# Kernel optimization log

Hardware: AMD Instinct MI355X
Metric: run time of the kernel (lower is better)

Reference implementation:

```python
import jax, jax.numpy as jnp
import numpy as np

V, E, H, W, S, T, B = 10000, 256, 512, 256, 512, 128, 64


def setup_inputs() -> dict:
    key = jax.random.key(0)
    ks = jax.random.split(key, 17)
    def rn(k, shape, s=0.08):
        return jax.random.normal(k, shape, jnp.float32) * s
    return {
        "tokens": jax.random.randint(ks[0], (B, S), 0, V),
        "dec_h0": jax.random.normal(ks[1], (B, H), jnp.float32),
        "emb_table": rn(ks[2], (V, E), 1.0),
        "enc_Wih": rn(ks[3], (4 * H, E)),
        "enc_Whh": rn(ks[4], (4 * H, H)),
        "enc_bih": rn(ks[5], (4 * H,)),
        "enc_bhh": rn(ks[6], (4 * H,)),
        "dec_Wih": rn(ks[7], (4 * H, E)),
        "dec_Whh": rn(ks[8], (4 * H, H)),
        "dec_bih": rn(ks[9], (4 * H,)),
        "dec_bhh": rn(ks[10], (4 * H,)),
        "W1_w": rn(ks[11], (W, H)),
        "W1_b": rn(ks[12], (W,)),
        "W2_w": rn(ks[13], (W, H)),
        "W2_b": rn(ks[14], (W,)),
        "vt_w": rn(ks[15], (1, W)),
        "vt_b": rn(ks[16], (1,)),
    }


def _lstm_cell(x, h, c, Wih, Whh, bih, bhh):
    # PyTorch gate order: input, forget, cell(g), output
    gates = x @ Wih.T + h @ Whh.T + bih + bhh
    i, f, g, o = jnp.split(gates, 4, axis=-1)
    c = jax.nn.sigmoid(f) * c + jax.nn.sigmoid(i) * jnp.tanh(g)
    h = jax.nn.sigmoid(o) * jnp.tanh(c)
    return h, c


def reference(tokens, dec_h0, emb_table, enc_Wih, enc_Whh, enc_bih, enc_bhh,
              dec_Wih, dec_Whh, dec_bih, dec_bhh, W1_w, W1_b, W2_w, W2_b,
              vt_w, vt_b):
    emb = emb_table[tokens]                       # [B,S,E]
    x_sbe = jnp.swapaxes(emb, 0, 1)               # [S,B,E] time-major
    bsz = tokens.shape[0]
    h0 = jnp.zeros((bsz, enc_Whh.shape[1]), emb.dtype)

    def enc_step(carry, x):
        h, c = carry
        h, c = _lstm_cell(x, h, c, enc_Wih, enc_Whh, enc_bih, enc_bhh)
        return (h, c), h

    _, enc_states = jax.lax.scan(enc_step, (h0, h0), x_sbe)   # [S,B,H]

    # W1(encoder_states) is constant across decoder steps -> hoist it
    blend1 = enc_states @ W1_w.T + W1_b            # [S,B,W]
    c0 = enc_states[-1]                            # original uses last enc state as cell init
    dec_in = jnp.zeros((bsz, emb_table.shape[1]), emb.dtype)  # never updated in original

    def dec_step(carry, _):
        h, c = carry
        h, c = _lstm_cell(dec_in, h, c, dec_Wih, dec_Whh, dec_bih, dec_bhh)
        blend2 = h @ W2_w.T + W2_b                 # [B,W]
        u = (jnp.tanh(blend1 + blend2[None]) @ vt_w.T)[..., 0] + vt_b[0]  # [S,B]
        logp = jax.nn.log_softmax(u.T, axis=1)     # [B,S], softmax over seq positions
        return (h, c), logp

    _, probs = jax.lax.scan(dec_step, (dec_h0, c0), None, length=T)  # [T,B,S]
    return jnp.swapaxes(probs, 0, 1)               # [B,T,S]
```

## Files before the change

kernel.cpp:

```cpp
#include <hip/hip_runtime.h>
#include <hip/hip_bf16.h>
#include <cstdint>
#include <cstddef>

typedef __bf16 bf16_t;
typedef __bf16 bf16x8 __attribute__((ext_vector_type(8)));
typedef float  f32x4  __attribute__((ext_vector_type(4)));

#define NB 64
#define NS 512
#define NTD 128
#define NE 256
#define NH 512
#define NG 2048
#define NW 256

#define HSTEP_DW 16384u

__device__ __forceinline__ float sigm_f(float x) { return 1.f / (1.f + __expf(-x)); }
__device__ __forceinline__ float tanh_f(float x) {
  float e = __expf(2.f * x);
  return 1.f - 2.f / (e + 1.f);
}
__device__ __forceinline__ float bits2f(uint32_t b16) {
  uint32_t u = b16 << 16;
  return __builtin_bit_cast(float, u);
}
__device__ __forceinline__ uint32_t packh(float a, float b) {
  uint16_t lo = __builtin_bit_cast(uint16_t, (bf16_t)a);
  uint16_t hi = __builtin_bit_cast(uint16_t, (bf16_t)b);
  return (uint32_t)lo | ((uint32_t)hi << 16);
}
__device__ __forceinline__ uint32_t aload(const uint32_t* p) {
  return __hip_atomic_load(p, __ATOMIC_RELAXED, __HIP_MEMORY_SCOPE_AGENT);
}
__device__ __forceinline__ uint64_t aload64(const uint64_t* p) {
  return __hip_atomic_load(p, __ATOMIC_RELAXED, __HIP_MEMORY_SCOPE_AGENT);
}
__device__ __forceinline__ void astore(uint32_t* p, uint32_t v) {
  __hip_atomic_store(p, v, __ATOMIC_RELAXED, __HIP_MEMORY_SCOPE_AGENT);
}

__global__ __launch_bounds__(256) void pack_all(
    const float* __restrict__ s0, bf16_t* __restrict__ d0,
    const float* __restrict__ s1, bf16_t* __restrict__ d1,
    const float* __restrict__ s2, bf16_t* __restrict__ d2,
    const float* __restrict__ s3, bf16_t* __restrict__ d3,
    const float* __restrict__ s4, bf16_t* __restrict__ d4) {
  int blk = blockIdx.x;
  const float* src; bf16_t* dst; int K, idx;
  if (blk < 2048)       { src = s0; dst = d0; K = 256; idx = blk * 256 + threadIdx.x; }
  else if (blk < 6144)  { src = s1; dst = d1; K = 512; idx = (blk - 2048) * 256 + threadIdx.x; }
  else if (blk < 10240) { src = s2; dst = d2; K = 512; idx = (blk - 6144) * 256 + threadIdx.x; }
  else if (blk < 10752) { src = s3; dst = d3; K = 512; idx = (blk - 10240) * 256 + threadIdx.x; }
  else                  { src = s4; dst = d4; K = 512; idx = (blk - 10752) * 256 + threadIdx.x; }
  int n = idx / K, k = idx - n * K;
  int lane = (((k & 31) >> 3) << 4) | (n & 15);
  size_t o = ((((size_t)(n >> 4) * (K >> 5)) + (k >> 5)) * 64 + lane) * 8 + (k & 7);
  dst[o] = (bf16_t)src[idx];
}

__global__ __launch_bounds__(256) void gather_emb2(
    const int* __restrict__ tokens, const float* __restrict__ table,
    bf16_t* __restrict__ embfrag, const float* __restrict__ dec_h0,
    uint32_t* __restrict__ dec_hf0) {
  int blk = blockIdx.x;
  if (blk < 4096) {
    int idx = blk * 256 + threadIdx.x;
    int row = idx >> 5, e0 = (idx & 31) << 3;
    int b = row & 63, s = row >> 6;
    int tok = tokens[b * NS + s];
    const float4* p = (const float4*)(table + (size_t)tok * NE + e0);
    float4 v0 = p[0], v1 = p[1];
    bf16x8 v;
    v[0] = (bf16_t)v0.x; v[1] = (bf16_t)v0.y; v[2] = (bf16_t)v0.z; v[3] = (bf16_t)v0.w;
    v[4] = (bf16_t)v1.x; v[5] = (bf16_t)v1.y; v[6] = (bf16_t)v1.z; v[7] = (bf16_t)v1.w;
    int mt = row >> 4;
    int ks = e0 >> 5;
    int lane = (b & 15) | (((e0 >> 3) & 3) << 4);
    *(bf16x8*)(embfrag + ((size_t)(mt * 8 + ks) * 64 + lane) * 8) = v;
  } else {
    int idx = (blk - 4096) * 256 + threadIdx.x;
    int b = idx >> 8, jp = idx & 255;
    int j = jp * 2;
    float lo = dec_h0[(size_t)b * NH + j], hi = dec_h0[(size_t)b * NH + j + 1];
    int bg = b >> 4, bl = b & 15, ks = j >> 5;
    int lane = bl | (((j >> 3) & 3) << 4);
    dec_hf0[((size_t)bg * 16 + ks) * 256 + lane * 4 + ((j >> 1) & 3)] = packh(lo, hi);
  }
}

__global__ __launch_bounds__(256) void gemm_xih_st(const bf16_t* __restrict__ A,
                                                   const bf16_t* __restrict__ Bp,
                                                   bf16_t* __restrict__ out,
                                                   const float* __restrict__ b1,
                                                   const float* __restrict__ b2) {
  __shared__ bf16_t tile[16][68];
  const int KS = 8, MT = 16;
  int lane = threadIdx.x & 63, w = threadIdx.x >> 6;
  int nt = blockIdx.x * 4 + w;
  int mt0 = blockIdx.y * MT;
  bf16x8 bfr[KS];
  const bf16_t* bp = Bp + ((size_t)nt * KS * 64 + lane) * 8;
#pragma unroll
  for (int ks = 0; ks < KS; ++ks) bfr[ks] = *(const bf16x8*)(bp + (size_t)ks * 512);
  int col = (nt << 4) + (lane & 15);
  float bs = b1[col] + b2[col];
  int row0 = (lane >> 4) << 2;
  int rw = threadIdx.x >> 4, ch = threadIdx.x & 15;
  for (int m = 0; m < MT; ++m) {
    int mt = mt0 + m;
    const bf16_t* ap = A + (size_t)mt * (KS * 512) + lane * 8;
    f32x4 acc = {0.f, 0.f, 0.f, 0.f};
#pragma unroll
    for (int ks = 0; ks < KS; ++ks)
      acc = __builtin_amdgcn_mfma_f32_16x16x32_bf16(
          *(const bf16x8*)(ap + (size_t)ks * 512), bfr[ks], acc, 0, 0, 0);
#pragma unroll
    for (int r = 0; r < 4; ++r)
      tile[row0 + r][w * 16 + (lane & 15)] = (bf16_t)(acc[r] + bs);
    __syncthreads();
    ushort4 v = *(const ushort4*)&tile[rw][ch * 4];
    *(ushort4*)(out + (size_t)(mt * 16 + rw) * NG + blockIdx.x * 64 + ch * 4) = v;
    __syncthreads();
  }
}

__global__ __launch_bounds__(256) void gemm_blends(
    const bf16_t* __restrict__ encA, const bf16_t* __restrict__ W1p,
    const float* __restrict__ W1_b, bf16_t* __restrict__ blend1,
    const bf16_t* __restrict__ decA, const bf16_t* __restrict__ W2p,
    const float* __restrict__ W2_b, float* __restrict__ blend2) {
  union { bf16_t t16[16][68]; float t32[16][68]; } sm;
  __shared__ decltype(sm) tile;
  const int KS = 16;
  int lane = threadIdx.x & 63, w = threadIdx.x >> 6;
  int nt = blockIdx.x * 4 + w;
  bool is1 = blockIdx.y < 128;
  int mt0 = (is1 ? blockIdx.y : (blockIdx.y - 128)) * 16;
  const bf16_t* A  = is1 ? encA : decA;
  const bf16_t* Bp = is1 ? W1p : W2p;
  const float* bias = is1 ? W1_b : W2_b;
  bf16x8 bfr[KS];
  const bf16_t* bp = Bp + ((size_t)nt * KS * 64 + lane) * 8;
#pragma unroll
  for (int ks = 0; ks < KS; ++ks) bfr[ks] = *(const bf16x8*)(bp + (size_t)ks * 512);
  int col = (nt << 4) + (lane & 15);
  float bs = bias[col];
  int row0 = (lane >> 4) << 2;
  int rw = threadIdx.x >> 4, ch = threadIdx.x & 15;
  for (int m = 0; m < 16; ++m) {
    int mt = mt0 + m;
    const bf16_t* ap = A + (size_t)mt * (KS * 512) + lane * 8;
    f32x4 acc = {0.f, 0.f, 0.f, 0.f};
#pragma unroll
    for (int ks = 0; ks < KS; ++ks)
      acc = __builtin_amdgcn_mfma_f32_16x16x32_bf16(
          *(const bf16x8*)(ap + (size_t)ks * 512), bfr[ks], acc, 0, 0, 0);
    if (is1) {
#pragma unroll
      for (int r = 0; r < 4; ++r)
        tile.t16[row0 + r][w * 16 + (lane & 15)] = (bf16_t)(acc[r] + bs);
      __syncthreads();
      ushort4 v = *(const ushort4*)&tile.t16[rw][ch * 4];
      *(ushort4*)(blend1 + (size_t)(mt * 16 + rw) * NW + blockIdx.x * 64 + ch * 4) = v;
      __syncthreads();
    } else {
#pragma unroll
      for (int r = 0; r < 4; ++r)
        tile.t32[row0 + r][w * 16 + (lane & 15)] = acc[r] + bs;
      __syncthreads();
      float4 v = *(const float4*)&tile.t32[rw][ch * 4];
      *(float4*)(blend2 + (size_t)(mt * 16 + rw) * NW + blockIdx.x * 64 + ch * 4) = v;
      __syncthreads();
    }
  }
}

__global__ __launch_bounds__(256) void lstm_chain_enc(
    const bf16_t* __restrict__ Wp, const bf16_t* __restrict__ xih,
    uint32_t* __restrict__ hfrag, uint32_t* __restrict__ flags) {
  __shared__ bf16_t wlds[8 * 8192];
  __shared__ float gl[4][16][36];
  int tid = threadIdx.x, lane = tid & 63, wv = tid >> 6;
  int bg = blockIdx.x >> 4, slice = blockIdx.x & 15;

  for (int l = 0; l < 8; ++l) {
    int g = l >> 1, p = l & 1;
    const bf16_t* src = Wp + (size_t)(g * 32 + slice * 2 + p) * 8192;
    bf16_t* dst = wlds + (size_t)l * 8192;
    for (int i = tid; i < 1024; i += 256)
      *(bf16x8*)(dst + (size_t)i * 8) = *(const bf16x8*)(src + (size_t)i * 8);
  }

  int ub = tid >> 4, uj2 = tid & 15;
  int lane_f = ub | ((uj2 >> 2) << 4);
  float c0 = 0.f, c1 = 0.f;
  __syncthreads();

  const uint64_t* hq = (const uint64_t*)hfrag;
  uint32_t* fl = flags + bg * 16;

  for (int t = 0; t < NS; ++t) {
    uint32_t xd[4];
    {
      const uint32_t* xr = (const uint32_t*)xih +
          ((size_t)(t * 64 + bg * 16 + ub)) * 1024 + slice * 16 + uj2;
#pragma unroll
      for (int g = 0; g < 4; ++g) xd[g] = xr[(size_t)g * 256];
    }
    if (t > 0) {
      uint32_t tgt = (uint32_t)t;
      bool ok;
      do {
        uint32_t f = tgt;
        if (lane < 16 && lane != (uint32_t)slice) f = aload(fl + lane);
        ok = __all(f >= tgt);
      } while (!ok);
    }
    const uint64_t* hb = hq + ((size_t)t * 4 + bg) * 2048 + lane * 2;
    uint64_t aq[16][2];
#pragma unroll
    for (int ks = 0; ks < 16; ++ks) {
      aq[ks][0] = aload64(hb + (size_t)ks * 128);
      aq[ks][1] = aload64(hb + (size_t)ks * 128 + 1);
    }
    const bf16_t* wl = wlds + (size_t)(wv * 2) * 8192 + lane * 8;
    f32x4 acc0 = {0.f, 0.f, 0.f, 0.f}, acc1 = {0.f, 0.f, 0.f, 0.f};
#pragma unroll
    for (int ks = 0; ks < 16; ++ks) {
      union { uint64_t q[2]; bf16x8 v; } u;
      u.q[0] = aq[ks][0]; u.q[1] = aq[ks][1];
      acc0 = __builtin_amdgcn_mfma_f32_16x16x32_bf16(
          u.v, *(const bf16x8*)(wl + (size_t)ks * 512), acc0, 0, 0, 0);
      acc1 = __builtin_amdgcn_mfma_f32_16x16x32_bf16(
          u.v, *(const bf16x8*)(wl + 8192 + (size_t)ks * 512), acc1, 0, 0, 0);
    }
    int cc = lane & 15, rb = (lane >> 4) << 2;
#pragma unroll
    for (int r = 0; r < 4; ++r) {
      gl[wv][rb + r][cc] = acc0[r];
      gl[wv][rb + r][16 + cc] = acc1[r];
    }
    __syncthreads();

    float p[4][2];
#pragma unroll
    for (int g = 0; g < 4; ++g) {
      p[g][0] = gl[g][ub][uj2 * 2] + bits2f(xd[g] & 0xffffu);
      p[g][1] = gl[g][ub][uj2 * 2 + 1] + bits2f(xd[g] >> 16);
    }
    float i0 = sigm_f(p[0][0]), f0 = sigm_f(p[1][0]);
    float g0 = tanh_f(p[2][0]), o0 = sigm_f(p[3][0]);
    c0 = f0 * c0 + i0 * g0;
    float h0 = o0 * tanh_f(c0);
    float i1 = sigm_f(p[0][1]), f1 = sigm_f(p[1][1]);
    float g1 = tanh_f(p[2][1]), o1 = sigm_f(p[3][1]);
    c1 = f1 * c1 + i1 * g1;
    float h1 = o1 * tanh_f(c1);
    astore(hfrag + ((size_t)(t + 1) * 4 + bg) * 4096 +
               slice * 256 + lane_f * 4 + (uj2 & 3), packh(h0, h1));
    __syncthreads();
    if (tid == 0) astore(fl + slice, (uint32_t)(t + 1));
  }
}

__global__ __launch_bounds__(256) void lstm_chain_dec(
    const bf16_t* __restrict__ Wp, const float* __restrict__ bih,
    const float* __restrict__ bhh, uint32_t* __restrict__ hfrag,
    const uint32_t* __restrict__ c0frag, uint32_t* __restrict__ flags) {
  __shared__ bf16_t wlds[8 * 8192];
  __shared__ float gl[4][16][36];
  int tid = threadIdx.x, lane = tid & 63, wv = tid >> 6;
  int bg = blockIdx.x >> 4, slice = blockIdx.x & 15;

  for (int l = 0; l < 8; ++l) {
    int g = l >> 1, p = l & 1;
    const bf16_t* src = Wp + (size_t)(g * 32 + slice * 2 + p) * 8192;
    bf16_t* dst = wlds + (size_t)l * 8192;
    for (int i = tid; i < 1024; i += 256)
      *(bf16x8*)(dst + (size_t)i * 8) = *(const bf16x8*)(src + (size_t)i * 8);
  }
  int ub = tid >> 4, uj2 = tid & 15;
  int j_lo = slice * 32 + uj2 * 2;
  int lane_f = ub | ((uj2 >> 2) << 4);
  uint32_t d = c0frag[((size_t)bg * 16 + slice) * 256 + lane_f * 4 + (uj2 & 3)];
  float c0 = bits2f(d & 0xffffu), c1 = bits2f(d >> 16);
  float bsum[4][2];
#pragma unroll
  for (int g = 0; g < 4; ++g) {
    bsum[g][0] = bih[g * NH + j_lo] + bhh[g * NH + j_lo];
    bsum[g][1] = bih[g * NH + j_lo + 1] + bhh[g * NH + j_lo + 1];
  }
  __syncthreads();

  const uint64_t* hq = (const uint64_t*)hfrag;
  uint32_t* fl = flags + bg * 16;

  for (int t = 0; t < NTD; ++t) {
    if (t > 0) {
      uint32_t tgt = (uint32_t)t;
      bool ok;
      do {
        uint32_t f = tgt;
        if (lane < 16 && lane != (uint32_t)slice) f = aload(fl + lane);
        ok = __all(f >= tgt);
      } while (!ok);
    }
    const uint64_t* hb = hq + ((size_t)t * 4 + bg) * 2048 + lane * 2;
    uint64_t aq[16][2];
#pragma unroll
    for (int ks = 0; ks < 16; ++ks) {
      aq[ks][0] = aload64(hb + (size_t)ks * 128);
      aq[ks][1] = aload64(hb + (size_t)ks * 128 + 1);
    }
    const bf16_t* wl = wlds + (size_t)(wv * 2) * 8192 + lane * 8;
    f32x4 acc0 = {0.f, 0.f, 0.f, 0.f}, acc1 = {0.f, 0.f, 0.f, 0.f};
#pragma unroll
    for (int ks = 0; ks < 16; ++ks) {
      union { uint64_t q[2]; bf16x8 v; } u;
      u.q[0] = aq[ks][0]; u.q[1] = aq[ks][1];
      acc0 = __builtin_amdgcn_mfma_f32_16x16x32_bf16(
          u.v, *(const bf16x8*)(wl + (size_t)ks * 512), acc0, 0, 0, 0);
      acc1 = __builtin_amdgcn_mfma_f32_16x16x32_bf16(
          u.v, *(const bf16x8*)(wl + 8192 + (size_t)ks * 512), acc1, 0, 0, 0);
    }
    int cc = lane & 15, rb = (lane >> 4) << 2;
#pragma unroll
    for (int r = 0; r < 4; ++r) {
      gl[wv][rb + r][cc] = acc0[r];
      gl[wv][rb + r][16 + cc] = acc1[r];
    }
    __syncthreads();

    float p[4][2];
#pragma unroll
    for (int g = 0; g < 4; ++g) {
      p[g][0] = gl[g][ub][uj2 * 2] + bsum[g][0];
      p[g][1] = gl[g][ub][uj2 * 2 + 1] + bsum[g][1];
    }
    float i0 = sigm_f(p[0][0]), f0 = sigm_f(p[1][0]);
    float g0 = tanh_f(p[2][0]), o0 = sigm_f(p[3][0]);
    c0 = f0 * c0 + i0 * g0;
    float h0 = o0 * tanh_f(c0);
    float i1 = sigm_f(p[0][1]), f1 = sigm_f(p[1][1]);
    float g1 = tanh_f(p[2][1]), o1 = sigm_f(p[3][1]);
    c1 = f1 * c1 + i1 * g1;
    float h1 = o1 * tanh_f(c1);
    astore(hfrag + ((size_t)(t + 1) * 4 + bg) * 4096 +
               slice * 256 + lane_f * 4 + (uj2 & 3), packh(h0, h1));
    __syncthreads();
    if (tid == 0) astore(fl + slice, (uint32_t)(t + 1));
  }
}

__global__ __launch_bounds__(256) void attn_v2(const bf16_t* __restrict__ blend1,
                                               const float* __restrict__ blend2,
                                               const float* __restrict__ vt_w,
                                               float* __restrict__ out) {
  __shared__ float s_u[512], s_red[8];
  int t = blockIdx.x >> 6, b = blockIdx.x & 63;
  int tid = threadIdx.x, lane = tid & 63, wv = tid >> 6;
  int sslot = lane >> 4, wseg = lane & 15;
  int w0 = wseg * 16;

  float vt[16], b2[16];
  {
    const float4* vp = (const float4*)(vt_w + w0);
    const float4* bp = (const float4*)(blend2 + (size_t)(t * 64 + b) * NW + w0);
#pragma unroll
    for (int i = 0; i < 4; ++i) {
      float4 a = vp[i], c = bp[i];
      vt[i * 4 + 0] = a.x; vt[i * 4 + 1] = a.y; vt[i * 4 + 2] = a.z; vt[i * 4 + 3] = a.w;
      b2[i * 4 + 0] = c.x; b2[i * 4 + 1] = c.y; b2[i * 4 + 2] = c.z; b2[i * 4 + 3] = c.w;
    }
  }
  for (int p = 0; p < 32; ++p) {
    int s = p * 16 + wv * 4 + sslot;
    const bf16_t* row = blend1 + ((size_t)s * NB + b) * NW + w0;
    bf16x8 v0 = *(const bf16x8*)(row);
    bf16x8 v1 = *(const bf16x8*)(row + 8);
    float val = 0.f;
#pragma unroll
    for (int k = 0; k < 8; ++k) val += vt[k] * tanh_f((float)v0[k] + b2[k]);
#pragma unroll
    for (int k = 0; k < 8; ++k) val += vt[8 + k] * tanh_f((float)v1[k] + b2[8 + k]);
    val += __shfl_xor(val, 1, 64);
    val += __shfl_xor(val, 2, 64);
    val += __shfl_xor(val, 4, 64);
    val += __shfl_xor(val, 8, 64);
    if (wseg == 0) s_u[s] = val;
  }
  __syncthreads();
  float a = s_u[tid], bb2 = s_u[tid + 256];
  float m = fmaxf(a, bb2);
#pragma unroll
  for (int o = 1; o < 64; o <<= 1) m = fmaxf(m, __shfl_xor(m, o, 64));
  if (lane == 0) s_red[wv] = m;
  __syncthreads();
  m = fmaxf(fmaxf(s_red[0], s_red[1]), fmaxf(s_red[2], s_red[3]));
  float e = __expf(a - m) + __expf(bb2 - m);
#pragma unroll
  for (int o = 1; o < 64; o <<= 1) e += __shfl_xor(e, o, 64);
  if (lane == 0) s_red[4 + wv] = e;
  __syncthreads();
  float lz = m + logf(s_red[4] + s_red[5] + s_red[6] + s_red[7]);
  size_t ob = ((size_t)b * NTD + t) * NS;
  out[ob + tid] = a - lz;
  out[ob + tid + 256] = bb2 - lz;
}

extern "C" void kernel_launch(void* const* d_in, const int* in_sizes, int n_in,
                              void* d_out, int out_size, void* d_ws, size_t ws_size,
                              hipStream_t stream) {
  const int*   tokens    = (const int*)d_in[0];
  const float* dec_h0    = (const float*)d_in[1];
  const float* emb_table = (const float*)d_in[2];
  const float* enc_Wih   = (const float*)d_in[3];
  const float* enc_Whh   = (const float*)d_in[4];
  const float* enc_bih   = (const float*)d_in[5];
  const float* enc_bhh   = (const float*)d_in[6];
  const float* dec_Whh   = (const float*)d_in[8];
  const float* dec_bih   = (const float*)d_in[9];
  const float* dec_bhh   = (const float*)d_in[10];
  const float* W1_w      = (const float*)d_in[11];
  const float* W1_b      = (const float*)d_in[12];
  const float* W2_w      = (const float*)d_in[13];
  const float* W2_b      = (const float*)d_in[14];
  const float* vt_w      = (const float*)d_in[15];
  float* out = (float*)d_out;

  char* w = (char*)d_ws;
  size_t off = 0;
  auto alloc = [&](size_t bytes) {
    size_t o = off;
    off += (bytes + 255) & ~(size_t)255;
    return o;
  };
  bf16_t* embfrag = (bf16_t*)(w + alloc((size_t)NS * NB * NE * 2));
  bf16_t* xih     = (bf16_t*)(w + alloc((size_t)NS * NB * NG * 2));
  uint32_t* enc_hf = (uint32_t*)(w + alloc((size_t)(NS + 1) * HSTEP_DW * 4));
  uint32_t* dec_hf = (uint32_t*)(w + alloc((size_t)(NTD + 1) * HSTEP_DW * 4));
  bf16_t* blend1  = (bf16_t*)(w + alloc((size_t)NS * NB * NW * 2));
  float*  blend2  = (float*)(w + alloc((size_t)NTD * NB * NW * 4));
  bf16_t* pWih    = (bf16_t*)(w + alloc((size_t)NG * NE * 2));
  bf16_t* pWhhE   = (bf16_t*)(w + alloc((size_t)NG * NH * 2));
  bf16_t* pWhhD   = (bf16_t*)(w + alloc((size_t)NG * NH * 2));
  bf16_t* pW1     = (bf16_t*)(w + alloc((size_t)NW * NH * 2));
  bf16_t* pW2     = (bf16_t*)(w + alloc((size_t)NW * NH * 2));
  uint32_t* flags = (uint32_t*)(w + alloc(512));
  (void)ws_size; (void)in_sizes; (void)n_in; (void)out_size;

  hipMemsetAsync(flags, 0, 512, stream);
  hipMemsetAsync(enc_hf, 0, HSTEP_DW * 4, stream);

  pack_all<<<11264, 256, 0, stream>>>(enc_Wih, pWih, enc_Whh, pWhhE,
                                      dec_Whh, pWhhD, W1_w, pW1, W2_w, pW2);

  gather_emb2<<<4160, 256, 0, stream>>>(tokens, emb_table, embfrag, dec_h0, dec_hf);

  gemm_xih_st<<<dim3(32, 128), 256, 0, stream>>>(embfrag, pWih, xih,
                                                 enc_bih, enc_bhh);

  lstm_chain_enc<<<64, 256, 0, stream>>>(pWhhE, xih, enc_hf, flags);

  lstm_chain_dec<<<64, 256, 0, stream>>>(pWhhD, dec_bih, dec_bhh, dec_hf,
                                         enc_hf + (size_t)NS * HSTEP_DW,
                                         flags + 64);

  gemm_blends<<<dim3(4, 160), 256, 0, stream>>>(
      (const bf16_t*)(enc_hf + HSTEP_DW), pW1, W1_b, blend1,
      (const bf16_t*)(dec_hf + HSTEP_DW), pW2, W2_b, blend2);

  attn_v2<<<NTD * NB, 256, 0, stream>>>(blend1, blend2, vt_w, out);
}
```

Baseline: 2.826 ms.

## Fuse encoder input projection into the LSTM recurrence kernel

```diff
diff --git a/kernel.cpp b/kernel.cpp
--- a/kernel.cpp
+++ b/kernel.cpp
@@ -90,49 +90,13 @@
   }
 }
 
-__global__ __launch_bounds__(256) void gemm_xih_st(const bf16_t* __restrict__ A,
-                                                   const bf16_t* __restrict__ Bp,
-                                                   bf16_t* __restrict__ out,
-                                                   const float* __restrict__ b1,
-                                                   const float* __restrict__ b2) {
-  __shared__ bf16_t tile[16][68];
-  const int KS = 8, MT = 16;
-  int lane = threadIdx.x & 63, w = threadIdx.x >> 6;
-  int nt = blockIdx.x * 4 + w;
-  int mt0 = blockIdx.y * MT;
-  bf16x8 bfr[KS];
-  const bf16_t* bp = Bp + ((size_t)nt * KS * 64 + lane) * 8;
-#pragma unroll
-  for (int ks = 0; ks < KS; ++ks) bfr[ks] = *(const bf16x8*)(bp + (size_t)ks * 512);
-  int col = (nt << 4) + (lane & 15);
-  float bs = b1[col] + b2[col];
-  int row0 = (lane >> 4) << 2;
-  int rw = threadIdx.x >> 4, ch = threadIdx.x & 15;
-  for (int m = 0; m < MT; ++m) {
-    int mt = mt0 + m;
-    const bf16_t* ap = A + (size_t)mt * (KS * 512) + lane * 8;
-    f32x4 acc = {0.f, 0.f, 0.f, 0.f};
-#pragma unroll
-    for (int ks = 0; ks < KS; ++ks)
-      acc = __builtin_amdgcn_mfma_f32_16x16x32_bf16(
-          *(const bf16x8*)(ap + (size_t)ks * 512), bfr[ks], acc, 0, 0, 0);
-#pragma unroll
-    for (int r = 0; r < 4; ++r)
-      tile[row0 + r][w * 16 + (lane & 15)] = (bf16_t)(acc[r] + bs);
-    __syncthreads();
-    ushort4 v = *(const ushort4*)&tile[rw][ch * 4];
-    *(ushort4*)(out + (size_t)(mt * 16 + rw) * NG + blockIdx.x * 64 + ch * 4) = v;
-    __syncthreads();
-  }
-}
-
 __global__ __launch_bounds__(256) void gemm_blends(
     const bf16_t* __restrict__ encA, const bf16_t* __restrict__ W1p,
     const float* __restrict__ W1_b, bf16_t* __restrict__ blend1,
     const bf16_t* __restrict__ decA, const bf16_t* __restrict__ W2p,
     const float* __restrict__ W2_b, float* __restrict__ blend2) {
-  union { bf16_t t16[16][68]; float t32[16][68]; } sm;
-  __shared__ decltype(sm) tile;
+  union SMU { bf16_t t16[16][68]; float t32[16][68]; };
+  __shared__ SMU tile;
   const int KS = 16;
   int lane = threadIdx.x & 63, w = threadIdx.x >> 6;
   int nt = blockIdx.x * 4 + w;
@@ -178,8 +142,10 @@
 }
 
 __global__ __launch_bounds__(256) void lstm_chain_enc(
-    const bf16_t* __restrict__ Wp, const bf16_t* __restrict__ xih,
-    uint32_t* __restrict__ hfrag, uint32_t* __restrict__ flags) {
+    const bf16_t* __restrict__ Wp, const bf16_t* __restrict__ Wihp,
+    const bf16_t* __restrict__ embfrag, const float* __restrict__ bih,
+    const float* __restrict__ bhh, uint32_t* __restrict__ hfrag,
+    uint32_t* __restrict__ flags) {
   __shared__ bf16_t wlds[8 * 8192];
   __shared__ float gl[4][16][36];
   int tid = threadIdx.x, lane = tid & 63, wv = tid >> 6;
@@ -192,23 +158,38 @@
     for (int i = tid; i < 1024; i += 256)
       *(bf16x8*)(dst + (size_t)i * 8) = *(const bf16x8*)(src + (size_t)i * 8);
   }
+  bf16x8 xf0[8], xf1[8];
+  {
+    int nt0 = wv * 32 + slice * 2;
+    const bf16_t* p0 = Wihp + (((size_t)nt0 * 8) * 64 + lane) * 8;
+    const bf16_t* p1 = Wihp + (((size_t)(nt0 + 1) * 8) * 64 + lane) * 8;
+#pragma unroll
+    for (int ks = 0; ks < 8; ++ks) {
+      xf0[ks] = *(const bf16x8*)(p0 + (size_t)ks * 512);
+      xf1[ks] = *(const bf16x8*)(p1 + (size_t)ks * 512);
+    }
+  }
 
   int ub = tid >> 4, uj2 = tid & 15;
+  int j_lo = slice * 32 + uj2 * 2;
   int lane_f = ub | ((uj2 >> 2) << 4);
   float c0 = 0.f, c1 = 0.f;
+  float bsum[4][2];
+#pragma unroll
+  for (int g = 0; g < 4; ++g) {
+    bsum[g][0] = bih[g * NH + j_lo] + bhh[g * NH + j_lo];
+    bsum[g][1] = bih[g * NH + j_lo + 1] + bhh[g * NH + j_lo + 1];
+  }
   __syncthreads();
 
   const uint64_t* hq = (const uint64_t*)hfrag;
   uint32_t* fl = flags + bg * 16;
 
   for (int t = 0; t < NS; ++t) {
-    uint32_t xd[4];
-    {
-      const uint32_t* xr = (const uint32_t*)xih +
-          ((size_t)(t * 64 + bg * 16 + ub)) * 1024 + slice * 16 + uj2;
-#pragma unroll
-      for (int g = 0; g < 4; ++g) xd[g] = xr[(size_t)g * 256];
-    }
+    bf16x8 ea[8];
+    const bf16_t* eb = embfrag + (((size_t)(t * 4 + bg) * 8) * 64 + lane) * 8;
+#pragma unroll
+    for (int ks = 0; ks < 8; ++ks) ea[ks] = *(const bf16x8*)(eb + (size_t)ks * 512);
     if (t > 0) {
       uint32_t tgt = (uint32_t)t;
       bool ok;
@@ -218,6 +199,12 @@
         ok = __all(f >= tgt);
       } while (!ok);
     }
+    f32x4 acc0 = {0.f, 0.f, 0.f, 0.f}, acc1 = {0.f, 0.f, 0.f, 0.f};
+#pragma unroll
+    for (int ks = 0; ks < 8; ++ks) {
+      acc0 = __builtin_amdgcn_mfma_f32_16x16x32_bf16(ea[ks], xf0[ks], acc0, 0, 0, 0);
+      acc1 = __builtin_amdgcn_mfma_f32_16x16x32_bf16(ea[ks], xf1[ks], acc1, 0, 0, 0);
+    }
     const uint64_t* hb = hq + ((size_t)t * 4 + bg) * 2048 + lane * 2;
     uint64_t aq[16][2];
 #pragma unroll
@@ -226,7 +213,6 @@
       aq[ks][1] = aload64(hb + (size_t)ks * 128 + 1);
     }
     const bf16_t* wl = wlds + (size_t)(wv * 2) * 8192 + lane * 8;
-    f32x4 acc0 = {0.f, 0.f, 0.f, 0.f}, acc1 = {0.f, 0.f, 0.f, 0.f};
 #pragma unroll
     for (int ks = 0; ks < 16; ++ks) {
       union { uint64_t q[2]; bf16x8 v; } u;
@@ -247,8 +233,8 @@
     float p[4][2];
 #pragma unroll
     for (int g = 0; g < 4; ++g) {
-      p[g][0] = gl[g][ub][uj2 * 2] + bits2f(xd[g] & 0xffffu);
-      p[g][1] = gl[g][ub][uj2 * 2 + 1] + bits2f(xd[g] >> 16);
+      p[g][0] = gl[g][ub][uj2 * 2] + bsum[g][0];
+      p[g][1] = gl[g][ub][uj2 * 2 + 1] + bsum[g][1];
     }
     float i0 = sigm_f(p[0][0]), f0 = sigm_f(p[1][0]);
     float g0 = tanh_f(p[2][0]), o0 = sigm_f(p[3][0]);
@@ -438,7 +424,6 @@
     return o;
   };
   bf16_t* embfrag = (bf16_t*)(w + alloc((size_t)NS * NB * NE * 2));
-  bf16_t* xih     = (bf16_t*)(w + alloc((size_t)NS * NB * NG * 2));
   uint32_t* enc_hf = (uint32_t*)(w + alloc((size_t)(NS + 1) * HSTEP_DW * 4));
   uint32_t* dec_hf = (uint32_t*)(w + alloc((size_t)(NTD + 1) * HSTEP_DW * 4));
   bf16_t* blend1  = (bf16_t*)(w + alloc((size_t)NS * NB * NW * 2));
@@ -459,10 +444,8 @@
 
   gather_emb2<<<4160, 256, 0, stream>>>(tokens, emb_table, embfrag, dec_h0, dec_hf);
 
-  gemm_xih_st<<<dim3(32, 128), 256, 0, stream>>>(embfrag, pWih, xih,
-                                                 enc_bih, enc_bhh);
-
-  lstm_chain_enc<<<64, 256, 0, stream>>>(pWhhE, xih, enc_hf, flags);
+  lstm_chain_enc<<<64, 256, 0, stream>>>(pWhhE, pWih, embfrag,
+                                         enc_bih, enc_bhh, enc_hf, flags);
 
   lstm_chain_dec<<<64, 256, 0, stream>>>(pWhhD, dec_bih, dec_bhh, dec_hf,
                                          enc_hf + (size_t)NS * HSTEP_DW,
```

Measured after the change: 2.668 ms, median of 2. -5.6%, faster.
